# Performance work log

Measured on AMD Instinct MI355X. Metric: run time of the kernel, lower is better.

The kernel has to match this reference:

```python
import jax, jax.numpy as jnp
import numpy as np

B, L, C, H = 1024, 64, 1024, 16  # windows*batch, window area, dim, heads
D = C // H  # head_dim = 64
WIN = 64  # window_size[0]; window_size = (64, 1)


def _relative_position_index():
    coords = np.arange(WIN)
    idx = coords[:, None] - coords[None, :] + (WIN - 1)
    return jnp.asarray(idx, dtype=jnp.int32)  # [L, L]


def setup_inputs() -> dict:
    key = jax.random.key(0)
    ks = jax.random.split(key, 8)
    s = 0.02
    return {
        "hidden_states": jax.random.normal(ks[0], (B, L, C), dtype=jnp.float32),
        "Wq": jax.random.normal(ks[1], (C, C), dtype=jnp.float32) * s,
        "bq": jax.random.normal(ks[2], (C,), dtype=jnp.float32) * s,
        "Wk": jax.random.normal(ks[3], (C, C), dtype=jnp.float32) * s,
        "bk": jax.random.normal(ks[4], (C,), dtype=jnp.float32) * s,
        "Wv": jax.random.normal(ks[5], (C, C), dtype=jnp.float32) * s,
        "bv": jax.random.normal(ks[6], (C,), dtype=jnp.float32) * s,
        "bias_table": jax.random.normal(ks[7], (2 * WIN - 1, H), dtype=jnp.float32) * s,
        "rel_index": _relative_position_index(),
    }


def reference(hidden_states, Wq, bq, Wk, bk, Wv, bv, bias_table, rel_index):
    b, l, c = hidden_states.shape
    # QKV projections -> [b, H, l, D]
    q = (hidden_states @ Wq + bq).reshape(b, l, H, D).transpose(0, 2, 1, 3)
    k = (hidden_states @ Wk + bk).reshape(b, l, H, D).transpose(0, 2, 1, 3)
    v = (hidden_states @ Wv + bv).reshape(b, l, H, D).transpose(0, 2, 1, 3)
    scores = jnp.einsum("bhqd,bhkd->bhqk", q, k) / jnp.sqrt(jnp.float32(D))
    # relative position bias: gather [L, L, H] -> [1, H, L, L]
    rel_bias = bias_table[rel_index]  # [L, L, H]
    scores = scores + rel_bias.transpose(2, 0, 1)[None]
    probs = jax.nn.softmax(scores, axis=-1)  # dropout p=0.0 (eval)
    context = jnp.einsum("bhqk,bhkd->bhqd", probs, v)
    context = context.transpose(0, 2, 1, 3).reshape(b, l, c)
    return context
```

## Files before the change

kernel.cpp:

```cpp
#include <hip/hip_runtime.h>
#include <hip/hip_fp16.h>
#include <stdint.h>

typedef _Float16 f16;
typedef _Float16 f16x8 __attribute__((ext_vector_type(8)));
typedef float f32x4 __attribute__((ext_vector_type(4)));

__device__ __forceinline__ void gload_lds16(const void* g, void* l) {
    __builtin_amdgcn_global_load_lds(
        (const __attribute__((address_space(1))) void*)g,
        (__attribute__((address_space(3))) void*)l,
        16, 0, 0);
}

__global__ __launch_bounds__(256) void convert_x(const float* __restrict__ X,
                                                 f16* __restrict__ Xh) {
    size_t i = ((size_t)blockIdx.x * 256 + threadIdx.x) * 8;
    float4 a = *(const float4*)(X + i);
    float4 b = *(const float4*)(X + i + 4);
    f16x8 o;
    o[0] = (f16)a.x; o[1] = (f16)a.y; o[2] = (f16)a.z; o[3] = (f16)a.w;
    o[4] = (f16)b.x; o[5] = (f16)b.y; o[6] = (f16)b.z; o[7] = (f16)b.w;
    *(f16x8*)(Xh + i) = o;
}

__global__ __launch_bounds__(1024) void transpose_w(const float* __restrict__ Wq,
                                                    const float* __restrict__ Wk,
                                                    const float* __restrict__ Wv,
                                                    f16* __restrict__ Wt) {
    __shared__ float tile[32][33];
    const int w = blockIdx.z;
    const float* W = (w == 0) ? Wq : ((w == 1) ? Wk : Wv);
    const int n0 = blockIdx.x * 32, k0 = blockIdx.y * 32;
    const int tx = threadIdx.x, ty = threadIdx.y;
    tile[ty][tx] = W[(size_t)(k0 + ty) * 1024 + n0 + tx];
    __syncthreads();
    Wt[(size_t)(w * 1024 + n0 + ty) * 1024 + k0 + tx] = (f16)tile[tx][ty];
}

__global__ __launch_bounds__(256) void qkv_gemm(const f16* __restrict__ A,
                                                const f16* __restrict__ Bt,
                                                const float* __restrict__ bq,
                                                const float* __restrict__ bk,
                                                const float* __restrict__ bv,
                                                f16* __restrict__ Out) {
    __shared__ __align__(16) f16 sA[128][32];
    __shared__ __align__(16) f16 sB[128][32];

    const int tid  = threadIdx.x;
    const int wave = tid >> 6, lane = tid & 63;
    const int quad = lane >> 4, l16 = lane & 15;
    const int m0 = blockIdx.y * 128, n0 = blockIdx.x * 128;
    const int wm = (wave & 1) * 64, wn = (wave >> 1) * 64;

    const int srow = lane >> 2;
    const int scol = (lane & 3) * 8;
    const f16* gA = A  + (size_t)(m0 + wave * 32 + srow) * 1024 + scol;
    const f16* gB = Bt + (size_t)(n0 + wave * 32 + srow) * 1024 + scol;
    f16* lA = &sA[wave * 32][0];
    f16* lB = &sB[wave * 32][0];

    f32x4 acc[4][4] = {};

    for (int k0 = 0; k0 < 1024; k0 += 32) {
        gload_lds16(gA + k0,             lA);
        gload_lds16(gA + k0 + 16 * 1024, lA + 16 * 32);
        gload_lds16(gB + k0,             lB);
        gload_lds16(gB + k0 + 16 * 1024, lB + 16 * 32);
        __syncthreads();

        f16x8 af[4], bf[4];
#pragma unroll
        for (int t = 0; t < 4; ++t)
            af[t] = *(const f16x8*)&sA[wm + t * 16 + l16][quad * 8];
#pragma unroll
        for (int t = 0; t < 4; ++t)
            bf[t] = *(const f16x8*)&sB[wn + t * 16 + l16][quad * 8];

#pragma unroll
        for (int mt = 0; mt < 4; ++mt)
#pragma unroll
            for (int nt = 0; nt < 4; ++nt)
                acc[mt][nt] = __builtin_amdgcn_mfma_f32_16x16x32_f16(
                    af[mt], bf[nt], acc[mt][nt], 0, 0, 0);
        __syncthreads();
    }

    const int w_idx = n0 >> 10;
    const float* bias = (w_idx == 0) ? bq : ((w_idx == 1) ? bk : bv);
    f16* out = Out + (size_t)w_idx * (65536UL * 1024UL);
#pragma unroll
    for (int mt = 0; mt < 4; ++mt) {
#pragma unroll
        for (int r = 0; r < 4; ++r) {
            const int m = m0 + wm + mt * 16 + quad * 4 + r;
            const int b = m >> 6, l = m & 63;
#pragma unroll
            for (int nt = 0; nt < 4; ++nt) {
                const int n  = n0 + wn + nt * 16 + l16;
                const int nc = n & 1023;
                const int h = nc >> 6, d = nc & 63;
                const float v = acc[mt][nt][r] + bias[nc];
                out[(((size_t)b * 16 + h) * 64 + l) * 64 + d] = (f16)v;
            }
        }
    }
}

__global__ __launch_bounds__(256) void attn(const f16* __restrict__ QKV,
                                            const float* __restrict__ bias_table,
                                            float* __restrict__ outp) {
    __shared__ __align__(16) f16 sQ[64][72];
    __shared__ __align__(16) f16 sK[64][72];
    __shared__ __align__(16) f16 sVt[64][72];
    __shared__ float sS[64][66];
    __shared__ float sR[64];

    const int bh = blockIdx.x;
    const int h  = bh & 15;
    const int tid  = threadIdx.x;
    const int wave = tid >> 6, lane = tid & 63;
    const int quad = lane >> 4, l16 = lane & 15;

    const f16* Qg = QKV + (size_t)bh * 4096;
    const f16* Kg = Qg + 65536UL * 1024UL;
    const f16* Vg = Kg + 65536UL * 1024UL;

#pragma unroll
    for (int j = 0; j < 2; ++j) {
        const int idx = tid + j * 256;
        const int e = idx * 8;
        const int l = e >> 6, d = e & 63;
        *(f16x8*)&sQ[l][d] = *(const f16x8*)(Qg + e);
        *(f16x8*)&sK[l][d] = *(const f16x8*)(Kg + e);
        f16x8 v = *(const f16x8*)(Vg + e);
#pragma unroll
        for (int i = 0; i < 8; ++i) sVt[d + i][l] = v[i];
    }
    __syncthreads();

    {
        f32x4 acc[4] = {};
#pragma unroll
        for (int k0 = 0; k0 < 64; k0 += 32) {
            f16x8 a = *(const f16x8*)&sQ[wave * 16 + l16][k0 + quad * 8];
#pragma unroll
            for (int nt = 0; nt < 4; ++nt) {
                f16x8 b = *(const f16x8*)&sK[nt * 16 + l16][k0 + quad * 8];
                acc[nt] = __builtin_amdgcn_mfma_f32_16x16x32_f16(a, b, acc[nt], 0, 0, 0);
            }
        }
#pragma unroll
        for (int nt = 0; nt < 4; ++nt) {
            const int jcol = nt * 16 + l16;
#pragma unroll
            for (int r = 0; r < 4; ++r) {
                const int i = wave * 16 + quad * 4 + r;
                const float bias = bias_table[(i - jcol + 63) * 16 + h];
                sS[i][jcol] = acc[nt][r] * 0.125f + bias;
            }
        }
    }
    __syncthreads();

    if (tid < 64) {
        float mx = -1e30f;
#pragma unroll
        for (int j = 0; j < 64; ++j) mx = fmaxf(mx, sS[tid][j]);
        float sum = 0.f;
#pragma unroll
        for (int j = 0; j < 64; ++j) {
            const float e = __expf(sS[tid][j] - mx);
            sum += e;
            sQ[tid][j] = (f16)e;
        }
        sR[tid] = 1.0f / sum;
    }
    __syncthreads();

    {
        f32x4 acc[4] = {};
#pragma unroll
        for (int k0 = 0; k0 < 64; k0 += 32) {
            f16x8 a = *(const f16x8*)&sQ[wave * 16 + l16][k0 + quad * 8];
#pragma unroll
            for (int nt = 0; nt < 4; ++nt) {
                f16x8 b = *(const f16x8*)&sVt[nt * 16 + l16][k0 + quad * 8];
                acc[nt] = __builtin_amdgcn_mfma_f32_16x16x32_f16(a, b, acc[nt], 0, 0, 0);
            }
        }
        const int b = bh >> 4;
#pragma unroll
        for (int nt = 0; nt < 4; ++nt) {
            const int d = nt * 16 + l16;
#pragma unroll
            for (int r = 0; r < 4; ++r) {
                const int i = wave * 16 + quad * 4 + r;
                outp[((size_t)b * 64 + i) * 1024 + h * 64 + d] = acc[nt][r] * sR[i];
            }
        }
    }
}

extern "C" void kernel_launch(void* const* d_in, const int* in_sizes, int n_in,
                              void* d_out, int out_size, void* d_ws, size_t ws_size,
                              hipStream_t stream) {
    const float* X          = (const float*)d_in[0];
    const float* Wq         = (const float*)d_in[1];
    const float* bq         = (const float*)d_in[2];
    const float* Wk         = (const float*)d_in[3];
    const float* bk         = (const float*)d_in[4];
    const float* Wv         = (const float*)d_in[5];
    const float* bv         = (const float*)d_in[6];
    const float* bias_table = (const float*)d_in[7];
    float* out = (float*)d_out;

    f16* Xh  = (f16*)d_ws;
    f16* Wt  = Xh + 67108864UL;
    f16* QKV = Wt + 3145728UL;

    convert_x<<<32768, 256, 0, stream>>>(X, Xh);
    transpose_w<<<dim3(32, 32, 3), dim3(32, 32), 0, stream>>>(Wq, Wk, Wv, Wt);
    qkv_gemm<<<dim3(24, 512), 256, 0, stream>>>(Xh, Wt, bq, bk, bv, QKV);
    attn<<<16384, 256, 0, stream>>>(QKV, bias_table, out);
}
```

Measured before the change: 1.125 ms.

## Store V pre-transposed from GEMM and do register-level softmax in attention

```diff
diff --git a/kernel.cpp b/kernel.cpp
--- a/kernel.cpp
+++ b/kernel.cpp
@@ -4,6 +4,7 @@
 
 typedef _Float16 f16;
 typedef _Float16 f16x8 __attribute__((ext_vector_type(8)));
+typedef _Float16 f16x4 __attribute__((ext_vector_type(4)));
 typedef float f32x4 __attribute__((ext_vector_type(4)));
 
 __device__ __forceinline__ void gload_lds16(const void* g, void* l) {
@@ -89,19 +90,38 @@
     const int w_idx = n0 >> 10;
     const float* bias = (w_idx == 0) ? bq : ((w_idx == 1) ? bk : bv);
     f16* out = Out + (size_t)w_idx * (65536UL * 1024UL);
-#pragma unroll
-    for (int mt = 0; mt < 4; ++mt) {
-#pragma unroll
-        for (int r = 0; r < 4; ++r) {
-            const int m = m0 + wm + mt * 16 + quad * 4 + r;
-            const int b = m >> 6, l = m & 63;
+    if (w_idx == 2) {
+#pragma unroll
+        for (int mt = 0; mt < 4; ++mt) {
+            const int mb = m0 + wm + mt * 16 + quad * 4;
+            const int b = mb >> 6, l0 = mb & 63;
 #pragma unroll
             for (int nt = 0; nt < 4; ++nt) {
                 const int n  = n0 + wn + nt * 16 + l16;
                 const int nc = n & 1023;
-                const int h = nc >> 6, d = nc & 63;
-                const float v = acc[mt][nt][r] + bias[nc];
-                out[(((size_t)b * 16 + h) * 64 + l) * 64 + d] = (f16)v;
+                const int hh = nc >> 6, d = nc & 63;
+                f16x4 pk;
+#pragma unroll
+                for (int r = 0; r < 4; ++r)
+                    pk[r] = (f16)(acc[mt][nt][r] + bias[nc]);
+                *(f16x4*)&out[(((size_t)b * 16 + hh) * 64 + d) * 64 + l0] = pk;
+            }
+        }
+    } else {
+#pragma unroll
+        for (int mt = 0; mt < 4; ++mt) {
+#pragma unroll
+            for (int r = 0; r < 4; ++r) {
+                const int m = m0 + wm + mt * 16 + quad * 4 + r;
+                const int b = m >> 6, l = m & 63;
+#pragma unroll
+                for (int nt = 0; nt < 4; ++nt) {
+                    const int n  = n0 + wn + nt * 16 + l16;
+                    const int nc = n & 1023;
+                    const int hh = nc >> 6, d = nc & 63;
+                    const float v = acc[mt][nt][r] + bias[nc];
+                    out[(((size_t)b * 16 + hh) * 64 + l) * 64 + d] = (f16)v;
+                }
             }
         }
     }
@@ -113,8 +133,8 @@
     __shared__ __align__(16) f16 sQ[64][72];
     __shared__ __align__(16) f16 sK[64][72];
     __shared__ __align__(16) f16 sVt[64][72];
-    __shared__ float sS[64][66];
-    __shared__ float sR[64];
+    __shared__ __align__(16) f16 sP[64][72];
+    __shared__ float sBias[128];
 
     const int bh = blockIdx.x;
     const int h  = bh & 15;
@@ -123,21 +143,24 @@
     const int quad = lane >> 4, l16 = lane & 15;
 
     const f16* Qg = QKV + (size_t)bh * 4096;
-    const f16* Kg = Qg + 65536UL * 1024UL;
-    const f16* Vg = Kg + 65536UL * 1024UL;
+    const f16* Kg = Qg + 67108864UL;
+    const f16* Vg = Kg + 67108864UL;
+
+    if (tid < 127) sBias[tid] = bias_table[tid * 16 + h];
 
 #pragma unroll
     for (int j = 0; j < 2; ++j) {
         const int idx = tid + j * 256;
         const int e = idx * 8;
-        const int l = e >> 6, d = e & 63;
-        *(f16x8*)&sQ[l][d] = *(const f16x8*)(Qg + e);
-        *(f16x8*)&sK[l][d] = *(const f16x8*)(Kg + e);
-        f16x8 v = *(const f16x8*)(Vg + e);
-#pragma unroll
-        for (int i = 0; i < 8; ++i) sVt[d + i][l] = v[i];
+        const int r0 = e >> 6, c0 = e & 63;
+        *(f16x8*)&sQ[r0][c0]  = *(const f16x8*)(Qg + e);
+        *(f16x8*)&sK[r0][c0]  = *(const f16x8*)(Kg + e);
+        *(f16x8*)&sVt[r0][c0] = *(const f16x8*)(Vg + e);
     }
     __syncthreads();
+
+    const int ib = wave * 16 + quad * 4;
+    float inv[4];
 
     {
         f32x4 acc[4] = {};
@@ -150,31 +173,44 @@
                 acc[nt] = __builtin_amdgcn_mfma_f32_16x16x32_f16(a, b, acc[nt], 0, 0, 0);
             }
         }
+        float sv[4][4];
+        float mx[4] = {-1e30f, -1e30f, -1e30f, -1e30f};
 #pragma unroll
         for (int nt = 0; nt < 4; ++nt) {
-            const int jcol = nt * 16 + l16;
+            const int j = nt * 16 + l16;
 #pragma unroll
             for (int r = 0; r < 4; ++r) {
-                const int i = wave * 16 + quad * 4 + r;
-                const float bias = bias_table[(i - jcol + 63) * 16 + h];
-                sS[i][jcol] = acc[nt][r] * 0.125f + bias;
-            }
-        }
-    }
-    __syncthreads();
-
-    if (tid < 64) {
-        float mx = -1e30f;
-#pragma unroll
-        for (int j = 0; j < 64; ++j) mx = fmaxf(mx, sS[tid][j]);
-        float sum = 0.f;
-#pragma unroll
-        for (int j = 0; j < 64; ++j) {
-            const float e = __expf(sS[tid][j] - mx);
-            sum += e;
-            sQ[tid][j] = (f16)e;
-        }
-        sR[tid] = 1.0f / sum;
+                const float s = acc[nt][r] * 0.125f + sBias[ib + r - j + 63];
+                sv[nt][r] = s;
+                mx[r] = fmaxf(mx[r], s);
+            }
+        }
+#pragma unroll
+        for (int off = 1; off < 16; off <<= 1)
+#pragma unroll
+            for (int r = 0; r < 4; ++r)
+                mx[r] = fmaxf(mx[r], __shfl_xor(mx[r], off));
+        float sum[4] = {0.f, 0.f, 0.f, 0.f};
+#pragma unroll
+        for (int nt = 0; nt < 4; ++nt)
+#pragma unroll
+            for (int r = 0; r < 4; ++r) {
+                const float e = __expf(sv[nt][r] - mx[r]);
+                sv[nt][r] = e;
+                sum[r] += e;
+            }
+#pragma unroll
+        for (int off = 1; off < 16; off <<= 1)
+#pragma unroll
+            for (int r = 0; r < 4; ++r)
+                sum[r] += __shfl_xor(sum[r], off);
+#pragma unroll
+        for (int r = 0; r < 4; ++r) inv[r] = 1.0f / sum[r];
+#pragma unroll
+        for (int nt = 0; nt < 4; ++nt)
+#pragma unroll
+            for (int r = 0; r < 4; ++r)
+                sP[ib + r][nt * 16 + l16] = (f16)sv[nt][r];
     }
     __syncthreads();
 
@@ -182,7 +218,7 @@
         f32x4 acc[4] = {};
 #pragma unroll
         for (int k0 = 0; k0 < 64; k0 += 32) {
-            f16x8 a = *(const f16x8*)&sQ[wave * 16 + l16][k0 + quad * 8];
+            f16x8 a = *(const f16x8*)&sP[wave * 16 + l16][k0 + quad * 8];
 #pragma unroll
             for (int nt = 0; nt < 4; ++nt) {
                 f16x8 b = *(const f16x8*)&sVt[nt * 16 + l16][k0 + quad * 8];
@@ -190,14 +226,13 @@
             }
         }
         const int b = bh >> 4;
+        float* op = outp + ((size_t)b * 64 + ib) * 1024 + h * 64;
 #pragma unroll
         for (int nt = 0; nt < 4; ++nt) {
             const int d = nt * 16 + l16;
 #pragma unroll
-            for (int r = 0; r < 4; ++r) {
-                const int i = wave * 16 + quad * 4 + r;
-                outp[((size_t)b * 64 + i) * 1024 + h * 64 + d] = acc[nt][r] * sR[i];
-            }
+            for (int r = 0; r < 4; ++r)
+                op[(size_t)r * 1024 + d] = acc[nt][r] * inv[r];
         }
     }
 }
```

New measurement: 1.071 ms. -4.8%, faster.
